# Performance work log

Measured on AMD Instinct MI355X. Metric: run time of the kernel, lower is better.

## Reference

```python
import jax, jax.numpy as jnp
import numpy as np
import math

EPS = 1e-5

def layernorm(x, w, b):
    mu = jnp.mean(x, axis=-1, keepdims=True)
    var = jnp.mean((x - mu) ** 2, axis=-1, keepdims=True)
    return (x - mu) / jnp.sqrt(var + EPS) * w + b

def pos_encoding(L, D):
    pos = jnp.arange(L, dtype=jnp.float32)[:, None]
    div = jnp.exp(jnp.arange(0, D, 2, dtype=jnp.float32) * (-math.log(10000.0) / D))
    pe = jnp.zeros((L, D), dtype=jnp.float32)
    pe = pe.at[:, 0::2].set(jnp.sin(pos * div))
    pe = pe.at[:, 1::2].set(jnp.cos(pos * div))
    return pe

def ssm_block(x, nw, nb, A, iw, ib, ow, ob):
    # x: [B,L,D]
    z = layernorm(x, nw, nb)
    proj = jnp.einsum('bld,ed->ble', z, iw) + ib  # [B,L,2D]
    u, g = jnp.split(proj, 2, axis=-1)
    g = jax.nn.sigmoid(g)
    u_t = jnp.swapaxes(u, 0, 1)  # [L,B,D]
    g_t = jnp.swapaxes(g, 0, 1)
    h0 = jnp.zeros(x.shape[::2], dtype=x.dtype)  # [B,D]
    def step(h, ug):
        ut, gt = ug
        h = gt * h + (1.0 - gt) * jnp.tanh(A * h + ut)
        return h, h
    _, hs = jax.lax.scan(step, h0, (u_t, g_t))  # hs: [L,B,D]
    out = jnp.einsum('lbd,ed->ble', hs, ow).swapaxes(0, 1).swapaxes(0, 1)
    out = jnp.einsum('lbd,ed->ble', hs, ow) + ob
    return x + out

def mha(x, qkv_w, qkv_b, ao_w, ao_b, nhead):
    B, L, D = x.shape
    dh = D // nhead
    qkv = jnp.einsum('bld,ed->ble', x, qkv_w) + qkv_b  # [B,L,3D]
    q, k, v = jnp.split(qkv, 3, axis=-1)
    def heads(t):
        return t.reshape(B, L, nhead, dh).transpose(0, 2, 1, 3)  # [B,H,L,dh]
    q, k, v = heads(q), heads(k), heads(v)
    scores = jnp.einsum('bhqd,bhkd->bhqk', q, k) / jnp.sqrt(jnp.asarray(dh, x.dtype))
    attn = jax.nn.softmax(scores, axis=-1)
    out = jnp.einsum('bhqk,bhkd->bhqd', attn, v)
    out = out.transpose(0, 2, 1, 3).reshape(B, L, D)
    return jnp.einsum('bld,ed->ble', out, ao_w) + ao_b

def encoder_layer(x, l1w, l1b, l2w, l2b, qkv_w, qkv_b, ao_w, ao_b, f1w, f1b, f2w, f2b, nhead):
    # norm_first pre-LN encoder layer, relu FFN, no dropout (eval)
    x = x + mha(layernorm(x, l1w, l1b), qkv_w, qkv_b, ao_w, ao_b, nhead)
    h = layernorm(x, l2w, l2b)
    h = jax.nn.relu(jnp.einsum('bld,fd->blf', h, f1w) + f1b)
    h = jnp.einsum('blf,df->bld', h, f2w) + f2b
    return x + h

def setup_inputs() -> dict:
    key = jax.random.key(0)
    ks = jax.random.split(key, 16)
    B, L, F, D, S, T = 8, 2048, 64, 128, 2, 2
    s = 0.05
    inp = {
        'x': jax.random.normal(ks[0], (B, L, F), jnp.float32),
        'in_w': jax.random.normal(ks[1], (D, F), jnp.float32) * s,
        'in_b': jnp.zeros((D,), jnp.float32),
        'ssm_norm_w': jnp.ones((S, D), jnp.float32),
        'ssm_norm_b': jnp.zeros((S, D), jnp.float32),
        'ssm_A': jax.random.normal(ks[2], (S, D), jnp.float32) * 0.1,
        'ssm_in_w': jax.random.normal(ks[3], (S, 2 * D, D), jnp.float32) * s,
        'ssm_in_b': jnp.zeros((S, 2 * D), jnp.float32),
        'ssm_out_w': jax.random.normal(ks[4], (S, D, D), jnp.float32) * s,
        'ssm_out_b': jnp.zeros((S, D), jnp.float32),
        'ln1_w': jnp.ones((T, D), jnp.float32),
        'ln1_b': jnp.zeros((T, D), jnp.float32),
        'ln2_w': jnp.ones((T, D), jnp.float32),
        'ln2_b': jnp.zeros((T, D), jnp.float32),
        'qkv_w': jax.random.normal(ks[5], (T, 3 * D, D), jnp.float32) * s,
        'qkv_b': jnp.zeros((T, 3 * D), jnp.float32),
        'ao_w': jax.random.normal(ks[6], (T, D, D), jnp.float32) * s,
        'ao_b': jnp.zeros((T, D), jnp.float32),
        'ff1_w': jax.random.normal(ks[7], (T, 4 * D, D), jnp.float32) * s,
        'ff1_b': jnp.zeros((T, 4 * D), jnp.float32),
        'ff2_w': jax.random.normal(ks[8], (T, D, 4 * D), jnp.float32) * s,
        'ff2_b': jnp.zeros((T, D), jnp.float32),
        'hln_w': jnp.ones((D,), jnp.float32),
        'hln_b': jnp.zeros((D,), jnp.float32),
        'h1_w': jax.random.normal(ks[9], (D, D), jnp.float32) * s,
        'h1_b': jnp.zeros((D,), jnp.float32),
        'h2_w': jax.random.normal(ks[10], (1, D), jnp.float32) * s,
        'h2_b': jnp.zeros((1,), jnp.float32),
    }
    return inp

NHEAD = 4

def reference(x, in_w, in_b, ssm_norm_w, ssm_norm_b, ssm_A, ssm_in_w, ssm_in_b,
              ssm_out_w, ssm_out_b, ln1_w, ln1_b, ln2_w, ln2_b, qkv_w, qkv_b,
              ao_w, ao_b, ff1_w, ff1_b, ff2_w, ff2_b, hln_w, hln_b, h1_w, h1_b,
              h2_w, h2_b):
    B, L, _ = x.shape
    D = in_w.shape[0]
    h = jnp.einsum('blf,df->bld', x, in_w) + in_b
    h = h + pos_encoding(L, D)[None]
    for i in range(ssm_A.shape[0]):
        h = ssm_block(h, ssm_norm_w[i], ssm_norm_b[i], ssm_A[i],
                      ssm_in_w[i], ssm_in_b[i], ssm_out_w[i], ssm_out_b[i])
    for i in range(ln1_w.shape[0]):
        h = encoder_layer(h, ln1_w[i], ln1_b[i], ln2_w[i], ln2_b[i],
                          qkv_w[i], qkv_b[i], ao_w[i], ao_b[i],
                          ff1_w[i], ff1_b[i], ff2_w[i], ff2_b[i], NHEAD)
    pooled = 0.5 * h[:, -1, :] + 0.5 * jnp.mean(h, axis=1)  # [B,D]
    p = layernorm(pooled, hln_w, hln_b)
    p = jax.nn.gelu(p @ h1_w.T + h1_b, approximate=False)
    return p @ h2_w.T + h2_b  # [B,1]
```

## Files before the change

### kernel.cpp

```cpp
#include <hip/hip_runtime.h>
#include <hip/hip_bf16.h>
#include <math.h>

#define L_SEQ 2048
#define D_MODEL 128
#define N_ROWS 16384
#define LOG2E 1.4426950408889634f

typedef __attribute__((ext_vector_type(8))) short bf16x8;
typedef __attribute__((ext_vector_type(4))) short short4v;
typedef __attribute__((ext_vector_type(4))) float f32x4;

__device__ __forceinline__ short f2bf(float x)
{
    __hip_bfloat16 b = __float2bfloat16(x);
    return *reinterpret_cast<short*>(&b);
}
__device__ __forceinline__ short f2bf_fast(float x)
{
    unsigned u = __builtin_bit_cast(unsigned, x);
    return (short)((u + 0x8000u) >> 16);
}
__device__ __forceinline__ float bf2f(short s)
{
    unsigned u = ((unsigned)(unsigned short)s) << 16;
    return __builtin_bit_cast(float, u);
}
__device__ __forceinline__ short f2h(float x)
{
    _Float16 h = (_Float16)x;
    return (short)__builtin_bit_cast(unsigned short, h);
}
__device__ __forceinline__ float h2f(short s)
{
    _Float16 h = __builtin_bit_cast(_Float16, (unsigned short)s);
    return (float)h;
}

__global__ __launch_bounds__(256) void convert_kernel(
    const float* __restrict__ x,    const float* __restrict__ inw,
    const float* __restrict__ ssmi, const float* __restrict__ ssmo,
    const float* __restrict__ qkvw, const float* __restrict__ aow,
    const float* __restrict__ f1w,  const float* __restrict__ f2w,
    short* __restrict__ xb, short* __restrict__ wb)
{
    int it = blockIdx.x * 256 + threadIdx.x;
    const float* src; short* dst; int off;
    if      (it < 131072) { src = x;    dst = xb;          off = it; }
    else if (it < 132096) { src = inw;  dst = wb;          off = it - 131072; }
    else if (it < 140288) { src = ssmi; dst = wb + 8192;   off = it - 132096; }
    else if (it < 144384) { src = ssmo; dst = wb + 73728;  off = it - 140288; }
    else if (it < 156672) { src = qkvw; dst = wb + 106496; off = it - 144384; }
    else if (it < 160768) { src = aow;  dst = wb + 204800; off = it - 156672; }
    else if (it < 177152) { src = f1w;  dst = wb + 237568; off = it - 160768; }
    else                  { src = f2w;  dst = wb + 368640; off = it - 177152; }
    off <<= 3;
    float4 v0 = *(const float4*)(src + off);
    float4 v1 = *(const float4*)(src + off + 4);
    bf16x8 p = {f2bf(v0.x), f2bf(v0.y), f2bf(v0.z), f2bf(v0.w),
                f2bf(v1.x), f2bf(v1.y), f2bf(v1.z), f2bf(v1.w)};
    *(bf16x8*)(dst + off) = p;
}

template <int FUSE>
__global__ __launch_bounds__(256) void gemm_ln(const short* __restrict__ A,
                                               const short* __restrict__ W,
                                               const float* __restrict__ bias,
                                               const float* __restrict__ lnw,
                                               const float* __restrict__ lnb,
                                               float* __restrict__ bh,
                                               short* __restrict__ lnout,
                                               int K)
{
    __shared__ __align__(16) short As[64][72];
    __shared__ __align__(16) short Bs[128][72];

    const int tid  = threadIdx.x;
    const int wave = tid >> 6;
    const int lane = tid & 63;
    const int m    = lane & 15;
    const int quad = lane >> 4;
    const int n0   = blockIdx.x * 64;

    const int arow = tid >> 2, acol = (tid & 3) << 4;
    const int brow = tid >> 1, bcol = (tid & 1) << 5;

    const short* Ap = A + (size_t)(n0 + arow) * K + acol;
    const short* Wp = W + (size_t)brow * K + bcol;

    f32x4 acc[8];
#pragma unroll
    for (int i = 0; i < 8; ++i) acc[i] = (f32x4){0.f, 0.f, 0.f, 0.f};

    bf16x8 a0 = *(const bf16x8*)Ap;
    bf16x8 a1 = *(const bf16x8*)(Ap + 8);
    bf16x8 b0 = *(const bf16x8*)Wp;
    bf16x8 b1 = *(const bf16x8*)(Wp + 8);
    bf16x8 b2 = *(const bf16x8*)(Wp + 16);
    bf16x8 b3 = *(const bf16x8*)(Wp + 24);

    for (int k0 = 0; k0 < K; k0 += 64) {
        *(bf16x8*)&As[arow][acol]      = a0;
        *(bf16x8*)&As[arow][acol + 8]  = a1;
        *(bf16x8*)&Bs[brow][bcol]      = b0;
        *(bf16x8*)&Bs[brow][bcol + 8]  = b1;
        *(bf16x8*)&Bs[brow][bcol + 16] = b2;
        *(bf16x8*)&Bs[brow][bcol + 24] = b3;
        __syncthreads();
        if (k0 + 64 < K) {
            a0 = *(const bf16x8*)(Ap + k0 + 64);
            a1 = *(const bf16x8*)(Ap + k0 + 72);
            b0 = *(const bf16x8*)(Wp + k0 + 64);
            b1 = *(const bf16x8*)(Wp + k0 + 72);
            b2 = *(const bf16x8*)(Wp + k0 + 80);
            b3 = *(const bf16x8*)(Wp + k0 + 88);
        }
#pragma unroll
        for (int ks = 0; ks < 2; ++ks) {
            bf16x8 af = *(const bf16x8*)&As[(wave << 4) + m][(ks << 5) + (quad << 3)];
#pragma unroll
            for (int nt = 0; nt < 8; ++nt) {
                bf16x8 bfr = *(const bf16x8*)&Bs[(nt << 4) + m][(ks << 5) + (quad << 3)];
                acc[nt] = __builtin_amdgcn_mfma_f32_16x16x32_bf16(af, bfr, acc[nt], 0, 0, 0);
            }
        }
        __syncthreads();
    }

#pragma unroll
    for (int nt = 0; nt < 8; ++nt) {
        int col = (nt << 4) + m;
        float bv = bias[col];
        float fr = 0.f;
        if (FUSE == 0)
            fr = __expf((float)(col & ~1) * (-0.07195578415606394f));
#pragma unroll
        for (int r = 0; r < 4; ++r) {
            int row = n0 + (wave << 4) + (quad << 2) + r;
            float t = acc[nt][r] + bv;
            if (FUSE == 0) {
                float ang = (float)(row & (L_SEQ - 1)) * fr;
                t += (col & 1) ? cosf(ang) : sinf(ang);
            } else {
                t += bh[(size_t)row * 128 + col];
            }
            acc[nt][r] = t;
            bh[(size_t)row * 128 + col] = t;
        }
    }

    if (FUSE < 2) {
        float wv[8], bvn[8];
#pragma unroll
        for (int nt = 0; nt < 8; ++nt) {
            wv[nt]  = lnw[(nt << 4) + m];
            bvn[nt] = lnb[(nt << 4) + m];
        }
#pragma unroll
        for (int r = 0; r < 4; ++r) {
            float s = 0.f;
#pragma unroll
            for (int nt = 0; nt < 8; ++nt) s += acc[nt][r];
            s += __shfl_xor(s, 1);
            s += __shfl_xor(s, 2);
            s += __shfl_xor(s, 4);
            s += __shfl_xor(s, 8);
            float mean = s * (1.f / 128.f);
            float q = 0.f;
#pragma unroll
            for (int nt = 0; nt < 8; ++nt) {
                float d = acc[nt][r] - mean;
                q = fmaf(d, d, q);
            }
            q += __shfl_xor(q, 1);
            q += __shfl_xor(q, 2);
            q += __shfl_xor(q, 4);
            q += __shfl_xor(q, 8);
            float inv = rsqrtf(q * (1.f / 128.f) + 1e-5f);
            int row = n0 + (wave << 4) + (quad << 2) + r;
#pragma unroll
            for (int nt = 0; nt < 8; ++nt) {
                int col = (nt << 4) + m;
                lnout[(size_t)row * 128 + col] =
                    f2bf((acc[nt][r] - mean) * inv * wv[nt] + bvn[nt]);
            }
        }
    }
}

enum { EPI_BF_RELU = 0, EPI_QKV = 1, EPI_SCAN_T = 2 };

template <int EPI>
__global__ __launch_bounds__(256) void gemm_bf(const short* __restrict__ A,
                                               const short* __restrict__ W,
                                               const float* __restrict__ bias,
                                               short* __restrict__ outb,
                                               short* __restrict__ outv,
                                               int K, int E)
{
    __shared__ __align__(16) short As[64][72];
    __shared__ __align__(16) short Bs[64][72];

    const int tid  = threadIdx.x;
    const int wave = tid >> 6;
    const int lane = tid & 63;
    const int m    = lane & 15;
    const int quad = lane >> 4;

    const int n0 = blockIdx.y * 64;
    const int e0 = blockIdx.x * 64;

    const int srow = tid >> 2;
    const int scol = (tid & 3) << 4;

    const short* Ap = A + (size_t)(n0 + srow) * K + scol;
    const short* Wp = W + (size_t)(e0 + srow) * K + scol;

    f32x4 acc[4];
#pragma unroll
    for (int i = 0; i < 4; ++i) acc[i] = (f32x4){0.f, 0.f, 0.f, 0.f};

    bf16x8 a0 = *(const bf16x8*)Ap;
    bf16x8 a1 = *(const bf16x8*)(Ap + 8);
    bf16x8 w0 = *(const bf16x8*)Wp;
    bf16x8 w1 = *(const bf16x8*)(Wp + 8);

    for (int k0 = 0; k0 < K; k0 += 64) {
        *(bf16x8*)&As[srow][scol]     = a0;
        *(bf16x8*)&As[srow][scol + 8] = a1;
        *(bf16x8*)&Bs[srow][scol]     = w0;
        *(bf16x8*)&Bs[srow][scol + 8] = w1;
        __syncthreads();
        if (k0 + 64 < K) {
            a0 = *(const bf16x8*)(Ap + k0 + 64);
            a1 = *(const bf16x8*)(Ap + k0 + 72);
            w0 = *(const bf16x8*)(Wp + k0 + 64);
            w1 = *(const bf16x8*)(Wp + k0 + 72);
        }
#pragma unroll
        for (int ks = 0; ks < 2; ++ks) {
            bf16x8 af = *(const bf16x8*)&As[(wave << 4) + m][(ks << 5) + (quad << 3)];
#pragma unroll
            for (int nt = 0; nt < 4; ++nt) {
                bf16x8 bfr = *(const bf16x8*)&Bs[(nt << 4) + m][(ks << 5) + (quad << 3)];
                acc[nt] = __builtin_amdgcn_mfma_f32_16x16x32_bf16(af, bfr, acc[nt], 0, 0, 0);
            }
        }
        __syncthreads();
    }

    if (EPI == EPI_QKV) {
        const float QSC = 0.17677669529663687f * LOG2E;
        if (e0 < 256) {
            short* dst = (e0 < 128) ? outb : (outb + 2097152);
            int cbase = (e0 < 128) ? e0 : (e0 - 128);
#pragma unroll
            for (int nt = 0; nt < 4; ++nt) {
                int col = cbase + (nt << 4) + m;
                float bv = bias[e0 + (nt << 4) + m];
#pragma unroll
                for (int r = 0; r < 4; ++r) {
                    int row = n0 + (wave << 4) + (quad << 2) + r;
                    float v = acc[nt][r] + bv;
                    if (e0 < 128) v *= QSC;
                    dst[(size_t)row * 128 + col] = f2bf(v);
                }
            }
        } else {
            int bb_ = n0 >> 11;
            int l0  = (n0 & (L_SEQ - 1)) + (wave << 4) + (quad << 2);
#pragma unroll
            for (int nt = 0; nt < 4; ++nt) {
                int c  = (e0 - 256) + (nt << 4) + m;
                int hh = c >> 5, dd = c & 31;
                float bv = bias[e0 + (nt << 4) + m];
                short4v pk;
#pragma unroll
                for (int r = 0; r < 4; ++r) pk[r] = f2bf(acc[nt][r] + bv);
                *(short4v*)&outv[(size_t)((bb_ * 4 + hh) * 32 + dd) * L_SEQ + l0] = pk;
            }
        }
    } else if (EPI == EPI_SCAN_T) {
        int bb_ = n0 >> 11;
        int l0  = (n0 & (L_SEQ - 1)) + (wave << 4) + (quad << 2);
#pragma unroll
        for (int nt = 0; nt < 4; ++nt) {
            int col = e0 + (nt << 4) + m;
            float bv = bias[col];
            short4v pk;
            if (e0 < 128) {
#pragma unroll
                for (int r = 0; r < 4; ++r)
                    pk[r] = f2h((acc[nt][r] + bv) * (2.f * LOG2E));
            } else {
#pragma unroll
                for (int r = 0; r < 4; ++r) {
                    float gr = acc[nt][r] + bv;
                    float g = __builtin_amdgcn_rcpf(
                        1.f + __builtin_amdgcn_exp2f(-gr * LOG2E));
                    pk[r] = f2h(g);
                }
            }
            *(short4v*)&outb[(((size_t)(bb_ * 256 + col)) << 11) + l0] = pk;
        }
    } else {
#pragma unroll
        for (int nt = 0; nt < 4; ++nt) {
            int col = e0 + (nt << 4) + m;
            float bv = bias[col];
#pragma unroll
            for (int r = 0; r < 4; ++r) {
                int row = n0 + (wave << 4) + (quad << 2) + r;
                float v = fmaxf(acc[nt][r] + bv, 0.f);
                outb[(size_t)row * E + col] = f2bf(v);
            }
        }
    }
}

#define SCAN_WARM 128

__device__ __forceinline__ void scan8(float& h, bf16x8 u8, bf16x8 g8,
                                      float a2, short* __restrict__ ob, int l0)
{
#pragma unroll
    for (int i = 0; i < 8; ++i) {
        float u2 = h2f(u8[i]);
        float g  = h2f(g8[i]);
        float omg = 1.f - g;
        float m2  = -2.f * omg;
        float c0 = fmaf(g, h, omg);
        float e2 = __builtin_amdgcn_exp2f(fmaf(a2, h, u2));
        float r  = __builtin_amdgcn_rcpf(1.f + e2);
        h = fmaf(m2, r, c0);
        ob[(l0 + i) * D_MODEL] = f2bf(h);
    }
}

__device__ __forceinline__ void scan8_ns(float& h, bf16x8 u8, bf16x8 g8,
                                         float a2)
{
#pragma unroll
    for (int i = 0; i < 8; ++i) {
        float u2 = h2f(u8[i]);
        float g  = h2f(g8[i]);
        float omg = 1.f - g;
        float m2  = -2.f * omg;
        float c0 = fmaf(g, h, omg);
        float e2 = __builtin_amdgcn_exp2f(fmaf(a2, h, u2));
        float r  = __builtin_amdgcn_rcpf(1.f + e2);
        h = fmaf(m2, r, c0);
    }
}

__global__ __launch_bounds__(64) void scan_kernel(const short* __restrict__ pt,
                                                  const float* __restrict__ A,
                                                  short* __restrict__ hs)
{
    int blk = blockIdx.x;
    int c   = blk & 15;
    int bd  = blk >> 4;
    int b   = bd >> 1;
    int d   = ((bd & 1) << 6) + threadIdx.x;
    float a2 = 2.f * A[d] * LOG2E;
    const short* up = pt + (((size_t)(b * 256 + d)) << 11);
    const short* gp = up + (((size_t)128) << 11);
    short* ob = hs + ((size_t)(b << 11)) * D_MODEL + d;

    const int lw = c << 7;
    float h = 0.f;

    bf16x8 uA0, uA1, gA0, gA1;

    if (c > 0) {
        int l0 = lw - SCAN_WARM;
        uA0 = *(const bf16x8*)(up + l0);
        uA1 = *(const bf16x8*)(up + l0 + 8);
        gA0 = *(const bf16x8*)(gp + l0);
        gA1 = *(const bf16x8*)(gp + l0 + 8);
        for (int l = l0; l < lw; l += 32) {
            bf16x8 uB0 = *(const bf16x8*)(up + l + 16);
            bf16x8 uB1 = *(const bf16x8*)(up + l + 24);
            bf16x8 gB0 = *(const bf16x8*)(gp + l + 16);
            bf16x8 gB1 = *(const bf16x8*)(gp + l + 24);
            scan8_ns(h, uA0, gA0, a2);
            scan8_ns(h, uA1, gA1, a2);
            uA0 = *(const bf16x8*)(up + l + 32);
            uA1 = *(const bf16x8*)(up + l + 40);
            gA0 = *(const bf16x8*)(gp + l + 32);
            gA1 = *(const bf16x8*)(gp + l + 40);
            scan8_ns(h, uB0, gB0, a2);
            scan8_ns(h, uB1, gB1, a2);
        }
    } else {
        uA0 = *(const bf16x8*)(up);
        uA1 = *(const bf16x8*)(up + 8);
        gA0 = *(const bf16x8*)(gp);
        gA1 = *(const bf16x8*)(gp + 8);
    }

    for (int l = lw; l < lw + 128; l += 32) {
        bf16x8 uB0 = *(const bf16x8*)(up + l + 16);
        bf16x8 uB1 = *(const bf16x8*)(up + l + 24);
        bf16x8 gB0 = *(const bf16x8*)(gp + l + 16);
        bf16x8 gB1 = *(const bf16x8*)(gp + l + 24);
        scan8(h, uA0, gA0, a2, ob, l);
        scan8(h, uA1, gA1, a2, ob, l + 8);
        if (l + 32 < lw + 128) {
            uA0 = *(const bf16x8*)(up + l + 32);
            uA1 = *(const bf16x8*)(up + l + 40);
            gA0 = *(const bf16x8*)(gp + l + 32);
            gA1 = *(const bf16x8*)(gp + l + 40);
        }
        scan8(h, uB0, gB0, a2, ob, l + 16);
        scan8(h, uB1, gB1, a2, ob, l + 24);
    }
}

__global__ __launch_bounds__(256) void attn_kernel(const short* __restrict__ Qs,
                                                   const short* __restrict__ Ks,
                                                   const short* __restrict__ Vtg,
                                                   short* __restrict__ outb)
{
    __shared__ __align__(16) short Klds[2][64][40];
    __shared__ __align__(16) short Vlds[2][32][72];
    __shared__ __align__(16) short Plds[4][16][72];

    const int tid  = threadIdx.x;
    const int wave = tid >> 6;
    const int lane = tid & 63;
    const int m    = lane & 15;
    const int quad = lane >> 4;

    const int bid = blockIdx.x;
    const int b  = bid >> 7;
    const int h  = (bid >> 5) & 3;
    const int q0 = (bid & 31) << 6;

    bf16x8 qfrag = *(const bf16x8*)&Qs[((size_t)((b << 11) + q0 + (wave << 4) + m)) * 128
                                       + (h << 5) + (quad << 3)];

    f32x4 O[2];
    O[0] = (f32x4){0.f, 0.f, 0.f, 0.f};
    O[1] = (f32x4){0.f, 0.f, 0.f, 0.f};
    float rs[4] = {0.f, 0.f, 0.f, 0.f};

    const int krow = tid >> 2, dg = (tid & 3) << 3;
    const int vrow = tid >> 3, kg = (tid & 7) << 3;
    const short* kbase = Ks + ((size_t)(b << 11) + krow) * 128 + (h << 5) + dg;
    const short* vbase = Vtg + ((size_t)((b << 2) + h) * 32 + vrow) * L_SEQ + kg;

    bf16x8 kreg = *(const bf16x8*)kbase;
    bf16x8 vreg = *(const bf16x8*)vbase;
    *(bf16x8*)&Klds[0][krow][dg] = kreg;
    *(bf16x8*)&Vlds[0][vrow][kg] = vreg;
    __syncthreads();

    for (int kc = 0; kc < 32; ++kc) {
        const int cur = kc & 1;
        if (kc < 31) {
            kreg = *(const bf16x8*)(kbase + (size_t)((kc + 1) << 6) * 128);
            vreg = *(const bf16x8*)(vbase + ((kc + 1) << 6));
        }

        f32x4 S[4];
#pragma unroll
        for (int kt = 0; kt < 4; ++kt) {
            bf16x8 kf = *(const bf16x8*)&Klds[cur][(kt << 4) + m][quad << 3];
            S[kt] = __builtin_amdgcn_mfma_f32_16x16x32_bf16(
                qfrag, kf, (f32x4){0.f, 0.f, 0.f, 0.f}, 0, 0, 0);
        }

#pragma unroll
        for (int kt = 0; kt < 4; ++kt)
#pragma unroll
            for (int r = 0; r < 4; ++r) {
                float p = __builtin_amdgcn_exp2f(S[kt][r]);
                rs[r] += p;
                Plds[wave][(quad << 2) + r][(kt << 4) + m] = f2bf_fast(p);
            }

#pragma unroll
        for (int ktile = 0; ktile < 2; ++ktile) {
            bf16x8 pf = *(const bf16x8*)&Plds[wave][m][(ktile << 5) + (quad << 3)];
#pragma unroll
            for (int dt = 0; dt < 2; ++dt) {
                bf16x8 vf = *(const bf16x8*)&Vlds[cur][(dt << 4) + m][(ktile << 5) + (quad << 3)];
                O[dt] = __builtin_amdgcn_mfma_f32_16x16x32_bf16(pf, vf, O[dt], 0, 0, 0);
            }
        }

        if (kc < 31) {
            *(bf16x8*)&Klds[cur ^ 1][krow][dg] = kreg;
            *(bf16x8*)&Vlds[cur ^ 1][vrow][kg] = vreg;
        }
        __syncthreads();
    }

#pragma unroll
    for (int r = 0; r < 4; ++r) {
        float s = rs[r];
        s += __shfl_xor(s, 1);
        s += __shfl_xor(s, 2);
        s += __shfl_xor(s, 4);
        s += __shfl_xor(s, 8);
        rs[r] = s;
    }

#pragma unroll
    for (int r = 0; r < 4; ++r) {
        float inv = 1.f / rs[r];
        int row = (b << 11) + q0 + (wave << 4) + (quad << 2) + r;
        short* op = outb + (size_t)row * D_MODEL + (h << 5) + m;
        op[0]  = f2bf(O[0][r] * inv);
        op[16] = f2bf(O[1][r] * inv);
    }
}

__global__ __launch_bounds__(1024) void pool_head_kernel(
    const float* __restrict__ h,
    const float* __restrict__ hlnw, const float* __restrict__ hlnb,
    const float* __restrict__ h1w, const float* __restrict__ h1b,
    const float* __restrict__ h2w, const float* __restrict__ h2b,
    float* __restrict__ out)
{
    __shared__ float part[8][128];
    __shared__ float sd[128];
    __shared__ float sq[128];

    int b   = blockIdx.x;
    int t   = threadIdx.x;
    int d   = t & 127;
    int seg = t >> 7;
    const float* hb = h + (size_t)b * L_SEQ * D_MODEL;

    float acc = 0.f;
    int l0 = seg << 8;
    for (int l = l0; l < l0 + 256; l += 4) {
        acc += hb[(l + 0) * D_MODEL + d] + hb[(l + 1) * D_MODEL + d]
             + hb[(l + 2) * D_MODEL + d] + hb[(l + 3) * D_MODEL + d];
    }
    part[seg][d] = acc;
    __syncthreads();

    float v = 0.f;
    if (t < 128) {
        float s = 0.f;
#pragma unroll
        for (int i = 0; i < 8; ++i) s += part[i][t];
        v = 0.5f * hb[(L_SEQ - 1) * D_MODEL + t] + 0.5f * (s * (1.f / (float)L_SEQ));
        sd[t] = v;
    }
    __syncthreads();
    for (int s = 64; s > 0; s >>= 1) {
        if (t < s) sd[t] += sd[t + s];
        __syncthreads();
    }
    float mu = sd[0] * (1.f / 128.f);
    __syncthreads();
    float dv = v - mu;
    if (t < 128) sd[t] = dv * dv;
    __syncthreads();
    for (int s = 64; s > 0; s >>= 1) {
        if (t < s) sd[t] += sd[t + s];
        __syncthreads();
    }
    float var = sd[0] * (1.f / 128.f);
    __syncthreads();
    if (t < 128) sq[t] = dv * rsqrtf(var + 1e-5f) * hlnw[t] + hlnb[t];
    __syncthreads();
    if (t < 128) {
        float dot = h1b[t];
        for (int d2 = 0; d2 < 128; ++d2) dot = fmaf(sq[d2], h1w[t * 128 + d2], dot);
        float ge = 0.5f * dot * (1.f + erff(dot * 0.7071067811865475f));
        sd[t] = ge * h2w[t];
    }
    __syncthreads();
    for (int s = 64; s > 0; s >>= 1) {
        if (t < s) sd[t] += sd[t + s];
        __syncthreads();
    }
    if (t == 0) out[b] = sd[0] + h2b[0];
}

extern "C" void kernel_launch(void* const* d_in, const int* in_sizes, int n_in,
                              void* d_out, int out_size, void* d_ws, size_t ws_size,
                              hipStream_t stream)
{
    (void)in_sizes; (void)n_in; (void)out_size; (void)ws_size;
    const float* x      = (const float*)d_in[0];
    const float* in_w   = (const float*)d_in[1];
    const float* in_b   = (const float*)d_in[2];
    const float* ssm_nw = (const float*)d_in[3];
    const float* ssm_nb = (const float*)d_in[4];
    const float* ssm_A  = (const float*)d_in[5];
    const float* ssm_iw = (const float*)d_in[6];
    const float* ssm_ib = (const float*)d_in[7];
    const float* ssm_ow = (const float*)d_in[8];
    const float* ssm_ob = (const float*)d_in[9];
    const float* ln1w   = (const float*)d_in[10];
    const float* ln1b   = (const float*)d_in[11];
    const float* ln2w   = (const float*)d_in[12];
    const float* ln2b   = (const float*)d_in[13];
    const float* qkvw   = (const float*)d_in[14];
    const float* qkvb   = (const float*)d_in[15];
    const float* aow    = (const float*)d_in[16];
    const float* aob    = (const float*)d_in[17];
    const float* f1w    = (const float*)d_in[18];
    const float* f1b    = (const float*)d_in[19];
    const float* f2w    = (const float*)d_in[20];
    const float* f2b    = (const float*)d_in[21];
    const float* hlnw   = (const float*)d_in[22];
    const float* hlnb   = (const float*)d_in[23];
    const float* h1w    = (const float*)d_in[24];
    const float* h1b    = (const float*)d_in[25];
    const float* h2w    = (const float*)d_in[26];
    const float* h2b    = (const float*)d_in[27];
    float* out = (float*)d_out;

    char* wsb = (char*)d_ws;
    float* bh     = (float*)(wsb);
    short* abuf   = (short*)(wsb + 8388608);
    short* bbuf   = (short*)(wsb + 25165824);
    short* qs     = (short*)(wsb + 29360128);
    short* vt     = (short*)(wsb + 37748736);
    short* xb     = (short*)(wsb + 41943040);
    short* wb     = (short*)(wsb + 44040192);
    short* ks     = qs + 2097152;

    dim3 blk(256);

    convert_kernel<<<756, blk, 0, stream>>>(x, in_w, ssm_iw, ssm_ow, qkvw, aow, f1w, f2w, xb, wb);

    gemm_ln<0><<<256, blk, 0, stream>>>(
        xb, wb, in_b, ssm_nw, ssm_nb, bh, bbuf, 64);

    gemm_bf<EPI_SCAN_T><<<dim3(4, 256), blk, 0, stream>>>(
        bbuf, wb + 8192, ssm_ib, abuf, nullptr, 128, 256);
    scan_kernel<<<256, 64, 0, stream>>>(abuf, ssm_A, bbuf);
    gemm_ln<1><<<256, blk, 0, stream>>>(
        bbuf, wb + 73728, ssm_ob, ssm_nw + 128, ssm_nb + 128, bh, bbuf, 128);

    gemm_bf<EPI_SCAN_T><<<dim3(4, 256), blk, 0, stream>>>(
        bbuf, wb + 8192 + 32768, ssm_ib + 256, abuf, nullptr, 128, 256);
    scan_kernel<<<256, 64, 0, stream>>>(abuf, ssm_A + 128, bbuf);
    gemm_ln<1><<<256, blk, 0, stream>>>(
        bbuf, wb + 73728 + 16384, ssm_ob + 128, ln1w, ln1b, bh, bbuf, 128);

    gemm_bf<EPI_QKV><<<dim3(6, 256), blk, 0, stream>>>(
        bbuf, wb + 106496, qkvb, qs, vt, 128, 384);
    attn_kernel<<<1024, blk, 0, stream>>>(qs, ks, vt, bbuf);
    gemm_ln<1><<<256, blk, 0, stream>>>(
        bbuf, wb + 204800, aob, ln2w, ln2b, bh, bbuf, 128);
    gemm_bf<EPI_BF_RELU><<<dim3(8, 256), blk, 0, stream>>>(
        bbuf, wb + 237568, f1b, abuf, nullptr, 128, 512);
    gemm_ln<1><<<256, blk, 0, stream>>>(
        abuf, wb + 368640, f2b, ln1w + 128, ln1b + 128, bh, bbuf, 512);

    gemm_bf<EPI_QKV><<<dim3(6, 256), blk, 0, stream>>>(
        bbuf, wb + 106496 + 49152, qkvb + 384, qs, vt, 128, 384);
    attn_kernel<<<1024, blk, 0, stream>>>(qs, ks, vt, bbuf);
    gemm_ln<1><<<256, blk, 0, stream>>>(
        bbuf, wb + 204800 + 16384, aob + 128, ln2w + 128, ln2b + 128, bh, bbuf, 128);
    gemm_bf<EPI_BF_RELU><<<dim3(8, 256), blk, 0, stream>>>(
        bbuf, wb + 237568 + 65536, f1b + 512, abuf, nullptr, 128, 512);
    gemm_ln<2><<<256, blk, 0, stream>>>(
        abuf, wb + 368640 + 65536, f2b + 128, nullptr, nullptr, bh, nullptr, 512);

    pool_head_kernel<<<8, 1024, 0, stream>>>(bh, hlnw, hlnb, h1w, h1b, h2w, h2b, out);
}
```

Baseline: 360.4 us.

## Load K/V fragments straight to registers in attention, drop LDS staging and barriers

The attention kernel no longer stages K and V tiles through shared memory with double buffering and per-chunk __syncthreads. Each wave now loads its own MFMA K/V fragments directly from global memory into double-buffered registers. It computes S transposed, with K as the A operand, so each lane writes its P values as one packed 4-element store and keeps a single row-sum scalar. Block indices are also remapped so that concurrently running blocks spread across batches and heads. This removes barriers and LDS traffic, but every wave in a block now reads the same K/V from global memory, four times the previous traffic, which relies on cache hits and adds register pressure.

```diff
diff --git a/kernel.cpp b/kernel.cpp
--- a/kernel.cpp
+++ b/kernel.cpp
@@ -422,8 +422,6 @@
                                                    const short* __restrict__ Vtg,
                                                    short* __restrict__ outb)
 {
-    __shared__ __align__(16) short Klds[2][64][40];
-    __shared__ __align__(16) short Vlds[2][32][72];
     __shared__ __align__(16) short Plds[4][16][72];
 
     const int tid  = threadIdx.x;
@@ -432,7 +430,8 @@
     const int m    = lane & 15;
     const int quad = lane >> 4;
 
-    const int bid = blockIdx.x;
+    const int raw = blockIdx.x;
+    const int bid = (raw & 7) * 128 + (raw >> 3);
     const int b  = bid >> 7;
     const int h  = (bid >> 5) & 3;
     const int q0 = (bid & 31) << 6;
@@ -443,73 +442,69 @@
     f32x4 O[2];
     O[0] = (f32x4){0.f, 0.f, 0.f, 0.f};
     O[1] = (f32x4){0.f, 0.f, 0.f, 0.f};
-    float rs[4] = {0.f, 0.f, 0.f, 0.f};
-
-    const int krow = tid >> 2, dg = (tid & 3) << 3;
-    const int vrow = tid >> 3, kg = (tid & 7) << 3;
-    const short* kbase = Ks + ((size_t)(b << 11) + krow) * 128 + (h << 5) + dg;
-    const short* vbase = Vtg + ((size_t)((b << 2) + h) * 32 + vrow) * L_SEQ + kg;
-
-    bf16x8 kreg = *(const bf16x8*)kbase;
-    bf16x8 vreg = *(const bf16x8*)vbase;
-    *(bf16x8*)&Klds[0][krow][dg] = kreg;
-    *(bf16x8*)&Vlds[0][vrow][kg] = vreg;
-    __syncthreads();
-
-    for (int kc = 0; kc < 32; ++kc) {
-        const int cur = kc & 1;
-        if (kc < 31) {
-            kreg = *(const bf16x8*)(kbase + (size_t)((kc + 1) << 6) * 128);
-            vreg = *(const bf16x8*)(vbase + ((kc + 1) << 6));
-        }
-
-        f32x4 S[4];
-#pragma unroll
-        for (int kt = 0; kt < 4; ++kt) {
-            bf16x8 kf = *(const bf16x8*)&Klds[cur][(kt << 4) + m][quad << 3];
-            S[kt] = __builtin_amdgcn_mfma_f32_16x16x32_bf16(
-                qfrag, kf, (f32x4){0.f, 0.f, 0.f, 0.f}, 0, 0, 0);
-        }
-
-#pragma unroll
-        for (int kt = 0; kt < 4; ++kt)
-#pragma unroll
-            for (int r = 0; r < 4; ++r) {
-                float p = __builtin_amdgcn_exp2f(S[kt][r]);
-                rs[r] += p;
-                Plds[wave][(quad << 2) + r][(kt << 4) + m] = f2bf_fast(p);
-            }
-
-#pragma unroll
-        for (int ktile = 0; ktile < 2; ++ktile) {
-            bf16x8 pf = *(const bf16x8*)&Plds[wave][m][(ktile << 5) + (quad << 3)];
-#pragma unroll
-            for (int dt = 0; dt < 2; ++dt) {
-                bf16x8 vf = *(const bf16x8*)&Vlds[cur][(dt << 4) + m][(ktile << 5) + (quad << 3)];
-                O[dt] = __builtin_amdgcn_mfma_f32_16x16x32_bf16(pf, vf, O[dt], 0, 0, 0);
-            }
-        }
-
-        if (kc < 31) {
-            *(bf16x8*)&Klds[cur ^ 1][krow][dg] = kreg;
-            *(bf16x8*)&Vlds[cur ^ 1][vrow][kg] = vreg;
-        }
-        __syncthreads();
-    }
+    float rs = 0.f;
+
+    const short* kbase = Ks + ((size_t)((b << 11) + m)) * 128 + (h << 5) + (quad << 3);
+    const short* vbase = Vtg + ((size_t)((b << 2) + h) * 32 + m) * L_SEQ + (quad << 3);
+
+    bf16x8 kA[4], vA[4], kB[4], vB[4];
+#pragma unroll
+    for (int kt = 0; kt < 4; ++kt)
+        kA[kt] = *(const bf16x8*)(kbase + (size_t)(kt << 4) * 128);
+    vA[0] = *(const bf16x8*)(vbase);
+    vA[1] = *(const bf16x8*)(vbase + 32);
+    vA[2] = *(const bf16x8*)(vbase + 16 * L_SEQ);
+    vA[3] = *(const bf16x8*)(vbase + 16 * L_SEQ + 32);
+
+#define ATTN_STEP(kc, CK, CV, NK, NV, DO_PF)                                    \
+    {                                                                           \
+        if (DO_PF) {                                                            \
+            const short* kn = kbase + (size_t)(((kc) + 1) << 6) * 128;          \
+            const short* vn = vbase + (((kc) + 1) << 6);                        \
+            _Pragma("unroll")                                                   \
+            for (int kt = 0; kt < 4; ++kt)                                      \
+                NK[kt] = *(const bf16x8*)(kn + (size_t)(kt << 4) * 128);        \
+            NV[0] = *(const bf16x8*)(vn);                                       \
+            NV[1] = *(const bf16x8*)(vn + 32);                                  \
+            NV[2] = *(const bf16x8*)(vn + 16 * L_SEQ);                          \
+            NV[3] = *(const bf16x8*)(vn + 16 * L_SEQ + 32);                     \
+        }                                                                       \
+        _Pragma("unroll")                                                       \
+        for (int kt = 0; kt < 4; ++kt) {                                        \
+            f32x4 S = __builtin_amdgcn_mfma_f32_16x16x32_bf16(                  \
+                CK[kt], qfrag, (f32x4){0.f, 0.f, 0.f, 0.f}, 0, 0, 0);           \
+            short4v pk;                                                         \
+            _Pragma("unroll")                                                   \
+            for (int r = 0; r < 4; ++r) {                                       \
+                float p = __builtin_amdgcn_exp2f(S[r]);                         \
+                rs += p;                                                        \
+                pk[r] = f2bf_fast(p);                                           \
+            }                                                                   \
+            *(short4v*)&Plds[wave][m][(kt << 4) + (quad << 2)] = pk;            \
+        }                                                                       \
+        _Pragma("unroll")                                                       \
+        for (int kt2 = 0; kt2 < 2; ++kt2) {                                     \
+            bf16x8 pf = *(const bf16x8*)&Plds[wave][m][(kt2 << 5) + (quad << 3)];\
+            _Pragma("unroll")                                                   \
+            for (int dt = 0; dt < 2; ++dt)                                      \
+                O[dt] = __builtin_amdgcn_mfma_f32_16x16x32_bf16(                \
+                    pf, CV[(dt << 1) | kt2], O[dt], 0, 0, 0);                   \
+        }                                                                       \
+    }
+
+    for (int kc = 0; kc < 32; kc += 2) {
+        ATTN_STEP(kc, kA, vA, kB, vB, 1);
+        ATTN_STEP(kc + 1, kB, vB, kA, vA, (kc + 2 < 32));
+    }
+#undef ATTN_STEP
+
+    rs += __shfl_xor(rs, 16);
+    rs += __shfl_xor(rs, 32);
 
 #pragma unroll
     for (int r = 0; r < 4; ++r) {
-        float s = rs[r];
-        s += __shfl_xor(s, 1);
-        s += __shfl_xor(s, 2);
-        s += __shfl_xor(s, 4);
-        s += __shfl_xor(s, 8);
-        rs[r] = s;
-    }
-
-#pragma unroll
-    for (int r = 0; r < 4; ++r) {
-        float inv = 1.f / rs[r];
+        float sv  = __shfl(rs, (quad << 2) + r);
+        float inv = 1.f / sv;
         int row = (b << 11) + q0 + (wave << 4) + (quad << 2) + r;
         short* op = outb + (size_t)row * D_MODEL + (h << 5) + m;
         op[0]  = f2bf(O[0][r] * inv);
```

Measured after the change: 503.9 us. +39.8%, slower.

## Transpose QK MFMA so P is stored as packed vectors, and remap block order

Applied to the files above, without the earlier changes.

Swaps the MFMA operand order in the attention kernel so each lane holds four keys for a single query row. The probabilities can then be packed into one 4-wide LDS store instead of four scalar strided stores, and the per-lane row sum becomes a single scalar reduced with two cross-quad shuffles. It also remaps the block index so consecutive workgroups interleave across batch/head groups, which may change cache/XCD locality. The change adds a shuffle per output row to fetch each row's sum.

```diff
diff --git a/kernel.cpp b/kernel.cpp
--- a/kernel.cpp
+++ b/kernel.cpp
@@ -432,7 +432,8 @@
     const int m    = lane & 15;
     const int quad = lane >> 4;
 
-    const int bid = blockIdx.x;
+    const int raw = blockIdx.x;
+    const int bid = (raw & 7) * 128 + (raw >> 3);
     const int b  = bid >> 7;
     const int h  = (bid >> 5) & 3;
     const int q0 = (bid & 31) << 6;
@@ -443,7 +444,7 @@
     f32x4 O[2];
     O[0] = (f32x4){0.f, 0.f, 0.f, 0.f};
     O[1] = (f32x4){0.f, 0.f, 0.f, 0.f};
-    float rs[4] = {0.f, 0.f, 0.f, 0.f};
+    float rs = 0.f;
 
     const int krow = tid >> 2, dg = (tid & 3) << 3;
     const int vrow = tid >> 3, kg = (tid & 7) << 3;
@@ -463,29 +464,27 @@
             vreg = *(const bf16x8*)(vbase + ((kc + 1) << 6));
         }
 
-        f32x4 S[4];
 #pragma unroll
         for (int kt = 0; kt < 4; ++kt) {
             bf16x8 kf = *(const bf16x8*)&Klds[cur][(kt << 4) + m][quad << 3];
-            S[kt] = __builtin_amdgcn_mfma_f32_16x16x32_bf16(
-                qfrag, kf, (f32x4){0.f, 0.f, 0.f, 0.f}, 0, 0, 0);
-        }
-
-#pragma unroll
-        for (int kt = 0; kt < 4; ++kt)
+            f32x4 S = __builtin_amdgcn_mfma_f32_16x16x32_bf16(
+                kf, qfrag, (f32x4){0.f, 0.f, 0.f, 0.f}, 0, 0, 0);
+            short4v pk;
 #pragma unroll
             for (int r = 0; r < 4; ++r) {
-                float p = __builtin_amdgcn_exp2f(S[kt][r]);
-                rs[r] += p;
-                Plds[wave][(quad << 2) + r][(kt << 4) + m] = f2bf_fast(p);
-            }
-
-#pragma unroll
-        for (int ktile = 0; ktile < 2; ++ktile) {
-            bf16x8 pf = *(const bf16x8*)&Plds[wave][m][(ktile << 5) + (quad << 3)];
+                float p = __builtin_amdgcn_exp2f(S[r]);
+                rs += p;
+                pk[r] = f2bf_fast(p);
+            }
+            *(short4v*)&Plds[wave][m][(kt << 4) + (quad << 2)] = pk;
+        }
+
+#pragma unroll
+        for (int kt2 = 0; kt2 < 2; ++kt2) {
+            bf16x8 pf = *(const bf16x8*)&Plds[wave][m][(kt2 << 5) + (quad << 3)];
 #pragma unroll
             for (int dt = 0; dt < 2; ++dt) {
-                bf16x8 vf = *(const bf16x8*)&Vlds[cur][(dt << 4) + m][(ktile << 5) + (quad << 3)];
+                bf16x8 vf = *(const bf16x8*)&Vlds[cur][(dt << 4) + m][(kt2 << 5) + (quad << 3)];
                 O[dt] = __builtin_amdgcn_mfma_f32_16x16x32_bf16(pf, vf, O[dt], 0, 0, 0);
             }
         }
@@ -497,19 +496,13 @@
         __syncthreads();
     }
 
+    rs += __shfl_xor(rs, 16);
+    rs += __shfl_xor(rs, 32);
+
 #pragma unroll
     for (int r = 0; r < 4; ++r) {
-        float s = rs[r];
-        s += __shfl_xor(s, 1);
-        s += __shfl_xor(s, 2);
-        s += __shfl_xor(s, 4);
-        s += __shfl_xor(s, 8);
-        rs[r] = s;
-    }
-
-#pragma unroll
-    for (int r = 0; r < 4; ++r) {
-        float inv = 1.f / rs[r];
+        float sv  = __shfl(rs, (quad << 2) + r);
+        float inv = 1.f / sv;
         int row = (b << 11) + q0 + (wave << 4) + (quad << 2) + r;
         short* op = outb + (size_t)row * D_MODEL + (h << 5) + m;
         op[0]  = f2bf(O[0][r] * inv);
```

Result: no change. 356.3 us (-1.1%).
